# Optimization experiments

Hardware: AMD Instinct MI355X
Metric: run time of the kernel (lower is better)

Reference implementation:

```python
import jax, jax.numpy as jnp
import numpy as np


def _circ_conv(x, K):
    # circular (wrap) padded cross-correlation, matching torch F.conv2d w/ circular pad
    p = K.shape[-1] // 2
    xp = jnp.pad(x, ((0, 0), (0, 0), (p, p), (p, p)), mode='wrap')
    return jax.lax.conv_general_dilated(xp, K, (1, 1), 'VALID',
                                        dimension_numbers=('NCHW', 'OIHW', 'NCHW'))


def _kernel_logdet(K, n):
    # log|det| of the block-circulant circular-conv operator via FFT of the kernel.
    # Mathematically identical to the Schur-complement spectral determinant used upstream.
    c, k = K.shape[0], K.shape[-1]
    Kp = jnp.zeros((c, c, n, n), dtype=K.dtype).at[:, :, :k, :k].set(K)
    Kh = jnp.fft.fft2(Kp)                       # (c, c, n, n) complex
    M = jnp.transpose(Kh, (2, 3, 0, 1))          # (n, n, c, c)
    _, logabs = jnp.linalg.slogdet(M)            # (n, n) real
    return jnp.sum(logabs).astype(K.dtype)


def setup_inputs() -> dict:
    key = jax.random.key(0)
    B, C, N, k, L = 512, 3, 128, 3, 3
    ks = jax.random.split(key, 7)
    x = jax.random.normal(ks[0], (B, C, N, N), dtype=jnp.float32)
    actnorm_bias = 0.1 * jax.random.normal(ks[1], (L, 1, C, 1, 1), dtype=jnp.float32)
    actnorm_log_scale = 0.1 * jax.random.normal(ks[2], (L, 1, C, 1, 1), dtype=jnp.float32)
    # identity kernel + 0.1 * he_uniform noise (as in the torch init)
    iden = jnp.zeros((C, C, k, k), dtype=jnp.float32).at[jnp.arange(C), jnp.arange(C), k // 2, k // 2].set(1.0)
    bound = float(np.sqrt(6.0 / (C * k * k)))
    conv_kernel = iden[None] + 0.1 * jax.random.uniform(ks[3], (L, C, C, k, k), minval=-bound, maxval=bound, dtype=jnp.float32)
    conv_bias = 0.01 * jax.random.normal(ks[4], (L, 1, C, N, N), dtype=jnp.float32)
    conv_log_scale = 0.01 * jax.random.normal(ks[5], (L, 1, C, N, N), dtype=jnp.float32)
    slog_log_alpha = 0.1 * jax.random.normal(ks[6], (L, 1, C, 1, 1), dtype=jnp.float32)
    return {'x': x, 'actnorm_bias': actnorm_bias, 'actnorm_log_scale': actnorm_log_scale,
            'conv_kernel': conv_kernel, 'conv_bias': conv_bias,
            'conv_log_scale': conv_log_scale, 'slog_log_alpha': slog_log_alpha}


def reference(x, actnorm_bias, actnorm_log_scale, conv_kernel, conv_bias, conv_log_scale, slog_log_alpha):
    n = x.shape[-1]
    L = conv_kernel.shape[0]
    total_logdet = jnp.zeros((x.shape[0],), dtype=x.dtype)
    h = x
    for i in range(L):  # small fixed layer count
        # actnorm
        ls = actnorm_log_scale[i]
        h = h * jnp.exp(ls) + actnorm_bias[i]
        total_logdet = total_logdet + (n * n) * jnp.sum(ls)
        # scaled circular conv + bias
        cls = conv_log_scale[i]
        h = jnp.exp(cls) * _circ_conv(h, conv_kernel[i]) + conv_bias[i]
        total_logdet = total_logdet + jnp.sum(cls) + _kernel_logdet(conv_kernel[i], n)
        # slog gate
        alpha = jnp.exp(slog_log_alpha[i])
        h = jnp.sign(h) / alpha * jnp.log1p(alpha * jnp.abs(h))
        total_logdet = total_logdet + jnp.sum(-alpha * jnp.abs(h), axis=(1, 2, 3))
    return h, total_logdet
```

## Files before the change

### kernel.cpp

```cpp
#include <hip/hip_runtime.h>

#define C_ 3
#define L_ 3
#define HB 38
#define WB 43
#define BUFSZ (C_*HB*WB)
#define NT   384

#define WS_LDPART 0
#define WS_LDC2   48
#define WS_W      64
#define WS_CC     320
#define WS_IALPHA 352
#define WS_LDACC  2048
#define WS_TAB    8192

#define TAB_CH    17408
#define TAB_ROW   136

__global__ void k_pre(const float* __restrict__ ab,
                      const float* __restrict__ als,
                      const float* __restrict__ K,
                      const float* __restrict__ la,
                      const float* __restrict__ cls,
                      const float* __restrict__ cb,
                      float* __restrict__ ws,
                      float2* __restrict__ tab, int B)
{
    __shared__ float sK[81];
    __shared__ float red[4];
    const int bid = blockIdx.x;
    const int t = threadIdx.x;

    if (bid < 612) {
        int idx = bid*256 + t;
        int ch  = idx / TAB_CH;
        int rem = idx - ch*TAB_CH;
        int y   = rem / TAB_ROW;
        int xp  = rem - y*TAB_ROW;
        int gx  = (xp - 3) & 127;
        float a = __expf(la[ch]);
        int src = ch*16384 + (y << 7) + gx;
        tab[idx] = make_float2(a*__expf(cls[src]), a*cb[src]);
        return;
    }
    if (bid < 660) {
        int lb  = bid - 612;
        int li  = lb >> 4;
        int sub = lb & 15;
        if (t < 81) sK[t] = K[li*81 + t];
        __syncthreads();
        float part = 0.f;
        {
            const float* p = cls + li*(3*128*128) + sub*3072;
            for (int i = t; i < 3072; i += 256) part += p[i];
        }
        const float w0 = -(2.f * 3.14159265358979f / 128.f);
        for (int f = sub*1024 + t; f < sub*1024 + 1024; f += 256) {
            int u = f >> 7, v = f & 127;
            float su, cu, sv, cv;
            __sincosf(w0 * (float)u, &su, &cu);
            __sincosf(w0 * (float)v, &sv, &cv);
            float cu2 = cu*cu - su*su, su2 = 2.f*cu*su;
            float cv2 = cv*cv - sv*sv, sv2 = 2.f*cv*sv;
            float evr[3] = {1.f, cv, cv2}, evi[3] = {0.f, sv, sv2};
            float eur[3] = {1.f, cu, cu2}, eui[3] = {0.f, su, su2};
            float Mr[3][3], Mi[3][3];
            #pragma unroll
            for (int o = 0; o < 3; ++o)
            #pragma unroll
            for (int i2 = 0; i2 < 3; ++i2) {
                float mr = 0.f, mi = 0.f;
                #pragma unroll
                for (int p = 0; p < 3; ++p) {
                    float rr = 0.f, ri = 0.f;
                    #pragma unroll
                    for (int q = 0; q < 3; ++q) {
                        float k = sK[(o*3+i2)*9 + p*3 + q];
                        rr += k * evr[q]; ri += k * evi[q];
                    }
                    mr += eur[p]*rr - eui[p]*ri;
                    mi += eur[p]*ri + eui[p]*rr;
                }
                Mr[o][i2] = mr; Mi[o][i2] = mi;
            }
            float c0r = (Mr[1][1]*Mr[2][2]-Mi[1][1]*Mi[2][2]) - (Mr[1][2]*Mr[2][1]-Mi[1][2]*Mi[2][1]);
            float c0i = (Mr[1][1]*Mi[2][2]+Mi[1][1]*Mr[2][2]) - (Mr[1][2]*Mi[2][1]+Mi[1][2]*Mr[2][1]);
            float c1r = (Mr[1][0]*Mr[2][2]-Mi[1][0]*Mi[2][2]) - (Mr[1][2]*Mr[2][0]-Mi[1][2]*Mi[2][0]);
            float c1i = (Mr[1][0]*Mi[2][2]+Mi[1][0]*Mr[2][2]) - (Mr[1][2]*Mi[2][0]+Mi[1][2]*Mr[2][0]);
            float c2r = (Mr[1][0]*Mr[2][1]-Mi[1][0]*Mi[2][1]) - (Mr[1][1]*Mr[2][0]-Mi[1][1]*Mi[2][0]);
            float c2i = (Mr[1][0]*Mi[2][1]+Mi[1][0]*Mr[2][1]) - (Mr[1][1]*Mi[2][0]+Mi[1][1]*Mr[2][0]);
            float dr = (Mr[0][0]*c0r-Mi[0][0]*c0i) - (Mr[0][1]*c1r-Mi[0][1]*c1i) + (Mr[0][2]*c2r-Mi[0][2]*c2i);
            float di = (Mr[0][0]*c0i+Mi[0][0]*c0r) - (Mr[0][1]*c1i+Mi[0][1]*c1r) + (Mr[0][2]*c2i+Mi[0][2]*c2r);
            part += 0.5f * __logf(dr*dr + di*di);
        }
        #pragma unroll
        for (int o = 32; o > 0; o >>= 1) part += __shfl_down(part, o, 64);
        if ((t & 63) == 0) red[t >> 6] = part;
        __syncthreads();
        if (t == 0) ws[WS_LDPART + lb] = red[0]+red[1]+red[2]+red[3];
        return;
    }
    for (int i = t; i < B; i += 256) ws[WS_LDACC + i] = 0.f;
    if (t < 243) {
        int li = t / 81; int rem = t % 81; int ic = (rem % 27) / 9;
        ws[WS_W + t] = K[t] * __expf(als[li*3 + ic]);
    }
    if (t < 9) {
        int li = t / 3, oc = t % 3;
        float s = 0.f;
        for (int ic = 0; ic < 3; ++ic) {
            float ks = 0.f;
            for (int k9 = 0; k9 < 9; ++k9) ks += K[((li*3+oc)*3+ic)*9 + k9];
            s += ab[li*3 + ic] * ks;
        }
        ws[WS_CC + t] = s;
        ws[WS_IALPHA + t] = __expf(-la[t]);
    }
    if (t == 9) {
        float s9 = 0.f;
        for (int i = 0; i < 9; ++i) s9 += als[i];
        ws[WS_LDC2] = 16384.f * s9;
    }
}

template<int S, bool FINAL>
static __device__ __forceinline__ void stage_fn(
    const float* src, float* dst,
    const float* __restrict__ ws, const float2* __restrict__ tab,
    int y0, int x0, float& ldpos, float* __restrict__ outb)
{
    constexpr int LI = S - 1;
    constexpr int W  = HB - 2*S;
    constexpr int QX = (W + 3) / 4;
    constexpr int Q  = W * QX;
    for (int q = threadIdx.x; q < Q; q += NT) {
        int qy  = q / QX;
        int iy  = S + qy;
        int ix0 = S + 4 * (q - qy*QX);
        float acc[3][4];
        #pragma unroll
        for (int oc = 0; oc < 3; ++oc) {
            float cc = ws[WS_CC + LI*3 + oc];
            acc[oc][0] = cc; acc[oc][1] = cc; acc[oc][2] = cc; acc[oc][3] = cc;
        }
        #pragma unroll
        for (int ic = 0; ic < 3; ++ic) {
            #pragma unroll
            for (int dy = 0; dy < 3; ++dy) {
                const float* rp = src + (ic*HB + iy - 1 + dy)*WB + ix0 - 1;
                float r[6];
                #pragma unroll
                for (int k = 0; k < 6; ++k) r[k] = rp[k];
                #pragma unroll
                for (int oc = 0; oc < 3; ++oc) {
                    #pragma unroll
                    for (int dx = 0; dx < 3; ++dx) {
                        float w = ws[WS_W + ((LI*3+oc)*3 + ic)*9 + dy*3 + dx];
                        #pragma unroll
                        for (int j = 0; j < 4; ++j) acc[oc][j] = fmaf(w, r[dx + j], acc[oc][j]);
                    }
                }
            }
        }
        int gy = (y0 + iy - 3) & 127;
        bool rowin = (iy >= 3 && iy < 35);
        const float2* tp0 = tab + LI*3*TAB_CH + gy*TAB_ROW + x0 + ix0;
        #pragma unroll
        for (int oc = 0; oc < 3; ++oc) {
            float ia = ws[WS_IALPHA + LI*3 + oc];
            const float2* tp = tp0 + oc*TAB_CH;
            float hv[4];
            #pragma unroll
            for (int j = 0; j < 4; ++j) {
                float2 tc = tp[j];
                float u  = fmaf(tc.x, acc[oc][j], tc.y);
                float lg = __logf(1.f + fabsf(u));
                hv[j] = copysignf(lg * ia, u);
                bool in = FINAL || (rowin && (unsigned)(ix0 + j - 3) < 32u);
                if (in) ldpos += lg;
            }
            if constexpr (FINAL) {
                int gyo = y0 + iy - 3, gxo = x0 + ix0 - 3;
                float4 pk;
                pk.x = hv[0]; pk.y = hv[1]; pk.z = hv[2]; pk.w = hv[3];
                *reinterpret_cast<float4*>(outb + ((oc << 14) + (gyo << 7) + gxo)) = pk;
            } else {
                float* dp = dst + (oc*HB + iy)*WB + ix0;
                dp[0] = hv[0]; dp[1] = hv[1]; dp[2] = hv[2]; dp[3] = hv[3];
            }
        }
    }
}

__global__ __launch_bounds__(NT, 6)
void k_main(const float* __restrict__ x,
            const float* __restrict__ ws,
            const float2* __restrict__ tab,
            float* ldacc,
            float* __restrict__ outh)
{
    __shared__ float Sb[2][BUFSZ];
    __shared__ float red[NT/64];
    int t = threadIdx.x;
    int b    = blockIdx.x >> 4;
    int tile = blockIdx.x & 15;
    int y0 = (tile >> 2) << 5, x0 = (tile & 3) << 5;

    if (t < 228) Sb[1][(t >> 1)*WB + 37 + (t & 1)] = 0.f;

    const float* xb = x + (size_t)b * 49152;
    for (int i = t; i < 768; i += NT) {
        int c = i >> 8, r = i & 255, iyr = r >> 3, ixq = (r & 7) << 2;
        float4 v = *reinterpret_cast<const float4*>(xb + c*16384 + ((y0 + iyr) << 7) + x0 + ixq);
        float* dp = &Sb[0][(c*HB + iyr + 3)*WB + 3 + ixq];
        dp[0] = v.x; dp[1] = v.y; dp[2] = v.z; dp[3] = v.w;
    }
    for (int i = t; i < 1260; i += NT) {
        int c = i / 420; int r = i - c*420;
        int iy, ix;
        if (r < 228) { iy = r / 38; ix = r - iy*38; if (iy >= 3) iy += 32; }
        else { int s2 = r - 228; int row = s2 / 6; int k = s2 - row*6;
               iy = 3 + row; ix = (k < 3) ? k : k + 32; }
        int gy = (y0 + iy - 3) & 127, gx = (x0 + ix - 3) & 127;
        Sb[0][(c*HB + iy)*WB + ix] = xb[c*16384 + (gy << 7) + gx];
    }
    __syncthreads();
    float ldpos = 0.f;
    stage_fn<1, false>(Sb[0], Sb[1], ws, tab, y0, x0, ldpos, nullptr);
    __syncthreads();
    stage_fn<2, false>(Sb[1], Sb[0], ws, tab, y0, x0, ldpos, nullptr);
    __syncthreads();
    stage_fn<3, true >(Sb[0], nullptr, ws, tab, y0, x0, ldpos,
                       outh + (size_t)b * 49152);
    #pragma unroll
    for (int o = 32; o > 0; o >>= 1) ldpos += __shfl_down(ldpos, o, 64);
    if ((t & 63) == 0) red[t >> 6] = ldpos;
    __syncthreads();
    if (t == 0) {
        float s = 0.f;
        #pragma unroll
        for (int wv = 0; wv < NT/64; ++wv) s += red[wv];
        atomicAdd(&ldacc[b], -s);
    }
}

__global__ void k_fin(const float* __restrict__ ws, float* __restrict__ outld, int B)
{
    int b = blockIdx.x * 256 + threadIdx.x;
    float c = ws[WS_LDC2];
    for (int i = 0; i < 48; ++i) c += ws[WS_LDPART + i];
    if (b < B) outld[b] = c + ws[WS_LDACC + b];
}

extern "C" void kernel_launch(void* const* d_in, const int* in_sizes, int n_in,
                              void* d_out, int out_size, void* d_ws, size_t ws_size,
                              hipStream_t stream)
{
    const float* x   = (const float*)d_in[0];
    const float* ab  = (const float*)d_in[1];
    const float* als = (const float*)d_in[2];
    const float* K   = (const float*)d_in[3];
    const float* cb  = (const float*)d_in[4];
    const float* cls = (const float*)d_in[5];
    const float* la  = (const float*)d_in[6];
    float* ws = (float*)d_ws;
    float* outh = (float*)d_out;
    float2* tab = (float2*)(ws + WS_TAB);

    const int B = in_sizes[0] / 49152;
    float* outld = outh + (size_t)B * 49152;

    k_pre <<<661,            256, 0, stream>>>(ab, als, K, la, cls, cb, ws, tab, B);
    k_main<<<B * 16,         NT,  0, stream>>>(x, ws, tab, ws + WS_LDACC, outh);
    k_fin <<<(B + 255)/256,  256, 0, stream>>>(ws, outld, B);
}
```

Baseline: 309.0 us.

## Compute two output rows per thread with packed FMA and duplicated weights

Each thread now handles a 2-row by 4-column output block instead of 1x4, packing the two rows into float2 vectors so the stencil runs through packed FMA on the element-wise fma builtin. Weights are stored duplicated and reordered in the workspace so a single vector load supplies both lanes. This aims to raise FMA throughput and reuse loaded input rows across two outputs. In exchange it needs more registers and the work per stage is split across fewer threads. W is always even (38-2S), so the row pairing covers every row.

```diff
diff --git a/kernel.cpp b/kernel.cpp
--- a/kernel.cpp
+++ b/kernel.cpp
@@ -1,4 +1,6 @@
 #include <hip/hip_runtime.h>
+
+typedef float f32x2 __attribute__((ext_vector_type(2)));
 
 #define C_ 3
 #define L_ 3
@@ -9,9 +11,9 @@
 
 #define WS_LDPART 0
 #define WS_LDC2   48
-#define WS_W      64
-#define WS_CC     320
-#define WS_IALPHA 352
+#define WS_CC     64
+#define WS_IALPHA 80
+#define WS_WD     96
 #define WS_LDACC  2048
 #define WS_TAB    8192
 
@@ -103,8 +105,11 @@
     }
     for (int i = t; i < B; i += 256) ws[WS_LDACC + i] = 0.f;
     if (t < 243) {
-        int li = t / 81; int rem = t % 81; int ic = (rem % 27) / 9;
-        ws[WS_W + t] = K[t] * __expf(als[li*3 + ic]);
+        int li = t / 81; int r1 = t % 81; int ic = r1 / 27; int r2 = r1 % 27;
+        int dy = r2 / 9; int r3 = r2 % 9; int oc = r3 / 3; int dx = r3 % 3;
+        float v = K[((li*3+oc)*3+ic)*9 + dy*3 + dx] * __expf(als[li*3 + ic]);
+        ws[WS_WD + 2*t    ] = v;
+        ws[WS_WD + 2*t + 1] = v;
     }
     if (t < 9) {
         int li = t / 3, oc = t % 3;
@@ -132,62 +137,81 @@
 {
     constexpr int LI = S - 1;
     constexpr int W  = HB - 2*S;
+    constexpr int PR = W / 2;
     constexpr int QX = (W + 3) / 4;
-    constexpr int Q  = W * QX;
-    for (int q = threadIdx.x; q < Q; q += NT) {
-        int qy  = q / QX;
-        int iy  = S + qy;
-        int ix0 = S + 4 * (q - qy*QX);
-        float acc[3][4];
+    constexpr int Q  = PR * QX;
+    const f32x2* __restrict__ wd = (const f32x2*)(ws + WS_WD);
+    for (int p = threadIdx.x; p < Q; p += NT) {
+        int pr  = p / QX;
+        int iy  = S + 2*pr;
+        int ix0 = S + 4*(p - pr*QX);
+        f32x2 acc[3][4];
         #pragma unroll
         for (int oc = 0; oc < 3; ++oc) {
             float cc = ws[WS_CC + LI*3 + oc];
-            acc[oc][0] = cc; acc[oc][1] = cc; acc[oc][2] = cc; acc[oc][3] = cc;
+            #pragma unroll
+            for (int c = 0; c < 4; ++c) acc[oc][c] = (f32x2){cc, cc};
         }
         #pragma unroll
         for (int ic = 0; ic < 3; ++ic) {
+            const float* bp = src + (ic*HB + iy - 1)*WB + ix0 - 1;
+            f32x2 P[3][6];
+            #pragma unroll
+            for (int dy = 0; dy < 3; ++dy)
+                #pragma unroll
+                for (int c = 0; c < 6; ++c)
+                    P[dy][c] = (f32x2){bp[dy*WB + c], bp[dy*WB + WB + c]};
             #pragma unroll
             for (int dy = 0; dy < 3; ++dy) {
-                const float* rp = src + (ic*HB + iy - 1 + dy)*WB + ix0 - 1;
-                float r[6];
-                #pragma unroll
-                for (int k = 0; k < 6; ++k) r[k] = rp[k];
+                const f32x2* wr = wd + ((LI*3 + ic)*3 + dy)*9;
                 #pragma unroll
                 for (int oc = 0; oc < 3; ++oc) {
                     #pragma unroll
                     for (int dx = 0; dx < 3; ++dx) {
-                        float w = ws[WS_W + ((LI*3+oc)*3 + ic)*9 + dy*3 + dx];
+                        f32x2 w = wr[oc*3 + dx];
                         #pragma unroll
-                        for (int j = 0; j < 4; ++j) acc[oc][j] = fmaf(w, r[dx + j], acc[oc][j]);
+                        for (int c = 0; c < 4; ++c)
+                            acc[oc][c] = __builtin_elementwise_fma(w, P[dy][dx + c], acc[oc][c]);
                     }
                 }
             }
         }
-        int gy = (y0 + iy - 3) & 127;
-        bool rowin = (iy >= 3 && iy < 35);
-        const float2* tp0 = tab + LI*3*TAB_CH + gy*TAB_ROW + x0 + ix0;
+        int gy0 = (y0 + iy - 3) & 127;
+        int gy1 = (y0 + iy - 2) & 127;
+        bool rin0 = (iy   >= 3 && iy   < 35);
+        bool rin1 = (iy+1 >= 3 && iy+1 < 35);
+        const int tbase = LI*3*TAB_CH + x0 + ix0;
         #pragma unroll
         for (int oc = 0; oc < 3; ++oc) {
             float ia = ws[WS_IALPHA + LI*3 + oc];
-            const float2* tp = tp0 + oc*TAB_CH;
-            float hv[4];
+            const float2* tpA = tab + tbase + oc*TAB_CH + gy0*TAB_ROW;
+            const float2* tpB = tab + tbase + oc*TAB_CH + gy1*TAB_ROW;
+            float hv0[4], hv1[4];
             #pragma unroll
             for (int j = 0; j < 4; ++j) {
-                float2 tc = tp[j];
-                float u  = fmaf(tc.x, acc[oc][j], tc.y);
-                float lg = __logf(1.f + fabsf(u));
-                hv[j] = copysignf(lg * ia, u);
-                bool in = FINAL || (rowin && (unsigned)(ix0 + j - 3) < 32u);
-                if (in) ldpos += lg;
+                bool colin = (unsigned)(ix0 + j - 3) < 32u;
+                float2 tA = tpA[j];
+                float u0  = fmaf(tA.x, acc[oc][j].x, tA.y);
+                float lg0 = __logf(1.f + fabsf(u0));
+                hv0[j] = copysignf(lg0 * ia, u0);
+                if (FINAL || (rin0 && colin)) ldpos += lg0;
+                float2 tB = tpB[j];
+                float u1  = fmaf(tB.x, acc[oc][j].y, tB.y);
+                float lg1 = __logf(1.f + fabsf(u1));
+                hv1[j] = copysignf(lg1 * ia, u1);
+                if (FINAL || (rin1 && colin)) ldpos += lg1;
             }
             if constexpr (FINAL) {
                 int gyo = y0 + iy - 3, gxo = x0 + ix0 - 3;
-                float4 pk;
-                pk.x = hv[0]; pk.y = hv[1]; pk.z = hv[2]; pk.w = hv[3];
-                *reinterpret_cast<float4*>(outb + ((oc << 14) + (gyo << 7) + gxo)) = pk;
+                float4 pk0, pk1;
+                pk0.x = hv0[0]; pk0.y = hv0[1]; pk0.z = hv0[2]; pk0.w = hv0[3];
+                pk1.x = hv1[0]; pk1.y = hv1[1]; pk1.z = hv1[2]; pk1.w = hv1[3];
+                *reinterpret_cast<float4*>(outb + ((oc << 14) + ( gyo      << 7) + gxo)) = pk0;
+                *reinterpret_cast<float4*>(outb + ((oc << 14) + ((gyo + 1) << 7) + gxo)) = pk1;
             } else {
                 float* dp = dst + (oc*HB + iy)*WB + ix0;
-                dp[0] = hv[0]; dp[1] = hv[1]; dp[2] = hv[2]; dp[3] = hv[3];
+                #pragma unroll
+                for (int j = 0; j < 4; ++j) { dp[j] = hv0[j]; dp[WB + j] = hv1[j]; }
             }
         }
     }
```

After: 341.6 us. 1.11x slower.
